# Kernel tuning notes

Hardware: AMD Instinct MI355X
Metric: run time of the kernel (lower is better)

Reference implementation:

```python
import jax, jax.numpy as jnp
import numpy as np

B, S, K, N = 4, 2048, 4096, 4096   # batch, seq, infeatures, outfeatures
GROUP = 128                        # quantization group size along K
N_OUT = 128                        # outlier features (last columns of x)


def setup_inputs() -> dict:
    key = jax.random.key(0)
    ks = jax.random.split(key, 6)
    x = jax.random.normal(ks[0], (B, S, K), dtype=jnp.float32)
    # unpacked 4-bit integer weights in [0, 16)
    qweight = jax.random.randint(ks[1], (N, K), 0, 16, dtype=jnp.int32)
    # per-group scales and scaled zeros: [numgroup, N] = [K//GROUP, N]
    scales = jax.random.uniform(ks[2], (K // GROUP, N), dtype=jnp.float32, minval=0.005, maxval=0.02)
    # scaled_zeros = -zeros * scales in the original pack(); keep them negative-ish
    scaled_zeros = -jax.random.uniform(ks[3], (K // GROUP, N), dtype=jnp.float32, minval=0.0, maxval=0.16)
    oweight = jax.random.normal(ks[4], (N, N_OUT), dtype=jnp.float32) * 0.02
    bias = jax.random.normal(ks[5], (N,), dtype=jnp.float32) * 0.02
    return {"x": x, "qweight": qweight, "scales": scales,
            "scaled_zeros": scaled_zeros, "oweight": oweight, "bias": bias}


def reference(x, qweight, scales, scaled_zeros, oweight, bias):
    # gemm_4bit: dequantize W[n,k] = q[n,k]*scales[k//G, n] + scaled_zeros[k//G, n]
    g = x.shape[-1] // scales.shape[0]
    scales_full = jnp.repeat(scales, g, axis=0).T        # [N, K]
    zeros_full = jnp.repeat(scaled_zeros, g, axis=0).T   # [N, K]
    W = qweight.astype(scales.dtype) * scales_full + zeros_full  # [N, K]
    y = jnp.einsum('bsk,nk->bsn', x, W)
    # fused outlier fp16 linear on the last N_OUT input features + bias
    n_out = oweight.shape[1]
    y = y + jnp.einsum('bso,no->bsn', x[..., -n_out:], oweight) + bias
    return y
```

## Files before the change

### kernel.cpp

```cpp
#include <hip/hip_runtime.h>

#define K_ 4096
#define N_ 4096
#define M_ 8192
#define NOUT_ 128

typedef __bf16 bf16x8 __attribute__((ext_vector_type(8)));
typedef float f32x4 __attribute__((ext_vector_type(4)));
typedef unsigned short ushort8 __attribute__((ext_vector_type(8)));

__device__ __forceinline__ unsigned short f2bf(float f) {
  unsigned u = __builtin_bit_cast(unsigned, f);
  u += 0x7fffu + ((u >> 16) & 1u);
  return (unsigned short)(u >> 16);
}

__global__ void cvt_x_kernel(const float4* __restrict__ x4, ushort8* __restrict__ xb) {
  const int t = blockIdx.x * 256 + threadIdx.x;
  float4 a = x4[2 * t];
  float4 b = x4[2 * t + 1];
  ushort8 o;
  o[0] = f2bf(a.x); o[1] = f2bf(a.y); o[2] = f2bf(a.z); o[3] = f2bf(a.w);
  o[4] = f2bf(b.x); o[5] = f2bf(b.y); o[6] = f2bf(b.z); o[7] = f2bf(b.w);
  xb[t] = o;
}

__global__ void dequant_kernel(const int4* __restrict__ q4,
                               const float* __restrict__ scales,
                               const float* __restrict__ zeros,
                               const float* __restrict__ ow,
                               ushort8* __restrict__ wb) {
  const int t = blockIdx.x * 256 + threadIdx.x;
  const int n = t >> 9;
  const int k = (t & 511) << 3;
  const int g = k >> 7;
  const float s = scales[g * N_ + n];
  const float z = zeros[g * N_ + n];
  int4 qa = q4[2 * t], qb = q4[2 * t + 1];
  float f[8];
  f[0] = qa.x * s + z; f[1] = qa.y * s + z; f[2] = qa.z * s + z; f[3] = qa.w * s + z;
  f[4] = qb.x * s + z; f[5] = qb.y * s + z; f[6] = qb.z * s + z; f[7] = qb.w * s + z;
  if (k >= K_ - NOUT_) {
    const float4* o4 = (const float4*)(ow + n * NOUT_ + (k - (K_ - NOUT_)));
    float4 oa = o4[0], ob = o4[1];
    f[0] += oa.x; f[1] += oa.y; f[2] += oa.z; f[3] += oa.w;
    f[4] += ob.x; f[5] += ob.y; f[6] += ob.z; f[7] += ob.w;
  }
  ushort8 r;
  #pragma unroll
  for (int i = 0; i < 8; ++i) r[i] = f2bf(f[i]);
  wb[t] = r;
}

__global__ __launch_bounds__(256, 3) void gemm_kernel(
    const unsigned short* __restrict__ xb,
    const unsigned short* __restrict__ wb,
    const float* __restrict__ bias,
    float* __restrict__ out) {
  __shared__ char sA[16384];
  __shared__ char sB[16384];

  const int tid  = threadIdx.x;
  const int w    = tid >> 6;
  const int lane = tid & 63;
  const int q    = lane >> 4;
  const int l16  = lane & 15;
  const int x7   = l16 & 7;
  const int wr   = w >> 1;
  const int wc   = w & 1;

  const int m0 = blockIdx.y * 128;
  const int n0 = blockIdx.x * 128;

  const unsigned short* gA[4];
  const unsigned short* gB[4];
  char* ldsA[4];
  char* ldsB[4];
  #pragma unroll
  for (int i = 0; i < 4; ++i) {
    const int o  = i * 4096 + w * 1024 + lane * 16;
    const int r  = o >> 7;
    const int cs = (o >> 4) & 7;
    const int cg = cs ^ (r & 7);
    gA[i] = xb + (size_t)(m0 + r) * K_ + cg * 8;
    gB[i] = wb + (size_t)(n0 + r) * K_ + cg * 8;
    ldsA[i] = sA + i * 4096 + w * 1024;
    ldsB[i] = sB + i * 4096 + w * 1024;
  }

  const char* pA = sA + (wr * 64 + l16) * 128;
  const char* pB = sB + (wc * 64 + l16) * 128;
  const int slot0 = ((0 + q) ^ x7) * 16;
  const int slot1 = ((4 + q) ^ x7) * 16;

  f32x4 acc[4][4] = {};

  for (int kt = 0; kt < K_ / 64; ++kt) {
    const int kof = kt * 64;
    #pragma unroll
    for (int i = 0; i < 4; ++i)
      __builtin_amdgcn_global_load_lds(
          (__attribute__((address_space(1))) void*)(gA[i] + kof),
          (__attribute__((address_space(3))) void*)ldsA[i], 16, 0, 0);
    #pragma unroll
    for (int i = 0; i < 4; ++i)
      __builtin_amdgcn_global_load_lds(
          (__attribute__((address_space(1))) void*)(gB[i] + kof),
          (__attribute__((address_space(3))) void*)ldsB[i], 16, 0, 0);
    __syncthreads();

    #pragma unroll
    for (int s = 0; s < 2; ++s) {
      const int slot = s ? slot1 : slot0;
      bf16x8 a[4], b[4];
      #pragma unroll
      for (int i = 0; i < 4; ++i)
        a[i] = *(const bf16x8*)(pA + i * 2048 + slot);
      #pragma unroll
      for (int j = 0; j < 4; ++j)
        b[j] = *(const bf16x8*)(pB + j * 2048 + slot);
      #pragma unroll
      for (int i = 0; i < 4; ++i)
        #pragma unroll
        for (int j = 0; j < 4; ++j)
          acc[i][j] = __builtin_amdgcn_mfma_f32_16x16x32_bf16(a[i], b[j], acc[i][j], 0, 0, 0);
    }
    __syncthreads();
  }

  float bv[4];
  #pragma unroll
  for (int j = 0; j < 4; ++j)
    bv[j] = bias[n0 + wc * 64 + j * 16 + l16];

  #pragma unroll
  for (int i = 0; i < 4; ++i) {
    const int mrow = m0 + wr * 64 + i * 16 + q * 4;
    #pragma unroll
    for (int j = 0; j < 4; ++j) {
      const int n = n0 + wc * 64 + j * 16 + l16;
      float* op = out + (size_t)mrow * N_ + n;
      #pragma unroll
      for (int r = 0; r < 4; ++r)
        op[(size_t)r * N_] = acc[i][j][r] + bv[j];
    }
  }
}

extern "C" void kernel_launch(void* const* d_in, const int* in_sizes, int n_in,
                              void* d_out, int out_size, void* d_ws, size_t ws_size,
                              hipStream_t stream) {
  const float* x      = (const float*)d_in[0];
  const int*   qw     = (const int*)d_in[1];
  const float* scales = (const float*)d_in[2];
  const float* zeros  = (const float*)d_in[3];
  const float* ow     = (const float*)d_in[4];
  const float* bias   = (const float*)d_in[5];
  float* out = (float*)d_out;

  unsigned short* xb = (unsigned short*)d_ws;
  unsigned short* wb = xb + (size_t)M_ * K_;

  cvt_x_kernel<<<(M_ * K_ / 8) / 256, 256, 0, stream>>>((const float4*)x, (ushort8*)xb);
  dequant_kernel<<<(N_ * K_ / 8) / 256, 256, 0, stream>>>((const int4*)qw, scales, zeros, ow,
                                                          (ushort8*)wb);
  dim3 grid(N_ / 128, M_ / 128);
  gemm_kernel<<<grid, 256, 0, stream>>>(xb, wb, bias, out);
}
```

Before: 531.6 us.

## Use 256x256 tiles with double-buffered LDS prefetch and 8-wave MFMA schedule

Tiles grow from 128x128 with 4 waves to 256x256 with 8 waves, and LDS becomes double-buffered so the next K-tile loads through global_load_lds while MFMAs run on the current one. The compute phase is split into four sub-phases separated by barriers and setprio hints, and block IDs are remapped for L2 locality. This targets global load latency and LDS traffic per MFMA. The cost is 128KB of LDS per block, which limits occupancy, more registers for the accumulators, and many extra barriers.

After: 552.5 us. 1.04x slower.

```diff
diff --git a/kernel.cpp b/kernel.cpp
--- a/kernel.cpp
+++ b/kernel.cpp
@@ -4,6 +4,7 @@
 #define N_ 4096
 #define M_ 8192
 #define NOUT_ 128
+#define NT_ (K_ / 64)
 
 typedef __bf16 bf16x8 __attribute__((ext_vector_type(8)));
 typedef float f32x4 __attribute__((ext_vector_type(4)));
@@ -52,80 +53,145 @@
   wb[t] = r;
 }
 
-__global__ __launch_bounds__(256, 3) void gemm_kernel(
+#define STAGE(dA, dB, kof)                                                          \
+  do {                                                                              \
+    _Pragma("unroll") for (int i_ = 0; i_ < 4; ++i_)                                \
+        __builtin_amdgcn_global_load_lds(                                           \
+            (__attribute__((address_space(1))) void*)(gA[i_] + (kof)),              \
+            (__attribute__((address_space(3))) void*)((dA) + aoff[i_]), 16, 0, 0);  \
+    _Pragma("unroll") for (int i_ = 0; i_ < 4; ++i_)                                \
+        __builtin_amdgcn_global_load_lds(                                           \
+            (__attribute__((address_space(1))) void*)(gB[i_] + (kof)),              \
+            (__attribute__((address_space(3))) void*)((dB) + aoff[i_]), 16, 0, 0);  \
+  } while (0)
+
+__global__ __launch_bounds__(512, 2) void gemm_kernel(
     const unsigned short* __restrict__ xb,
     const unsigned short* __restrict__ wb,
     const float* __restrict__ bias,
     float* __restrict__ out) {
-  __shared__ char sA[16384];
-  __shared__ char sB[16384];
+  __shared__ __attribute__((aligned(16))) char lds[131072];
 
   const int tid  = threadIdx.x;
   const int w    = tid >> 6;
   const int lane = tid & 63;
   const int q    = lane >> 4;
   const int l16  = lane & 15;
-  const int x7   = l16 & 7;
-  const int wr   = w >> 1;
-  const int wc   = w & 1;
-
-  const int m0 = blockIdx.y * 128;
-  const int n0 = blockIdx.x * 128;
+  const int wr   = w >> 2;
+  const int wc   = w & 3;
+
+  const int id  = blockIdx.y * 16 + blockIdx.x;
+  const int id2 = (id & 7) * 64 + (id >> 3);
+  const int m0  = (id2 >> 4) * 256;
+  const int n0  = (id2 & 15) * 256;
 
   const unsigned short* gA[4];
   const unsigned short* gB[4];
-  char* ldsA[4];
-  char* ldsB[4];
+  int aoff[4];
   #pragma unroll
   for (int i = 0; i < 4; ++i) {
-    const int o  = i * 4096 + w * 1024 + lane * 16;
+    const int o  = i * 8192 + w * 1024 + lane * 16;
     const int r  = o >> 7;
     const int cs = (o >> 4) & 7;
     const int cg = cs ^ (r & 7);
     gA[i] = xb + (size_t)(m0 + r) * K_ + cg * 8;
     gB[i] = wb + (size_t)(n0 + r) * K_ + cg * 8;
-    ldsA[i] = sA + i * 4096 + w * 1024;
-    ldsB[i] = sB + i * 4096 + w * 1024;
-  }
-
-  const char* pA = sA + (wr * 64 + l16) * 128;
-  const char* pB = sB + (wc * 64 + l16) * 128;
-  const int slot0 = ((0 + q) ^ x7) * 16;
-  const int slot1 = ((4 + q) ^ x7) * 16;
-
-  f32x4 acc[4][4] = {};
-
-  for (int kt = 0; kt < K_ / 64; ++kt) {
-    const int kof = kt * 64;
-    #pragma unroll
-    for (int i = 0; i < 4; ++i)
-      __builtin_amdgcn_global_load_lds(
-          (__attribute__((address_space(1))) void*)(gA[i] + kof),
-          (__attribute__((address_space(3))) void*)ldsA[i], 16, 0, 0);
-    #pragma unroll
-    for (int i = 0; i < 4; ++i)
-      __builtin_amdgcn_global_load_lds(
-          (__attribute__((address_space(1))) void*)(gB[i] + kof),
-          (__attribute__((address_space(3))) void*)ldsB[i], 16, 0, 0);
-    __syncthreads();
-
-    #pragma unroll
-    for (int s = 0; s < 2; ++s) {
-      const int slot = s ? slot1 : slot0;
-      bf16x8 a[4], b[4];
-      #pragma unroll
-      for (int i = 0; i < 4; ++i)
-        a[i] = *(const bf16x8*)(pA + i * 2048 + slot);
-      #pragma unroll
-      for (int j = 0; j < 4; ++j)
-        b[j] = *(const bf16x8*)(pB + j * 2048 + slot);
-      #pragma unroll
-      for (int i = 0; i < 4; ++i)
-        #pragma unroll
-        for (int j = 0; j < 4; ++j)
-          acc[i][j] = __builtin_amdgcn_mfma_f32_16x16x32_bf16(a[i], b[j], acc[i][j], 0, 0, 0);
-    }
-    __syncthreads();
+    aoff[i] = i * 8192 + w * 1024;
+  }
+
+  const char* pA0 = lds + (wr * 128 + l16) * 128;
+  const char* pB0 = lds + 65536 + (wc * 64 + l16) * 128;
+  const int sl0 = ((0 + q) ^ (l16 & 7)) * 16;
+  const int sl1 = ((4 + q) ^ (l16 & 7)) * 16;
+
+  f32x4 acc[8][4] = {};
+
+  STAGE((char*)lds, (char*)lds + 65536, 0);
+
+  for (int t = 0; t < NT_; ++t) {
+    const int curo = (t & 1) * 32768;
+    const char* cA = pA0 + curo;
+    const char* cB = pB0 + curo;
+
+    if (t + 1 < NT_) {
+      char* dA = (char*)lds + (((t + 1) & 1) * 32768);
+      char* dB = (char*)lds + 65536 + (((t + 1) & 1) * 32768);
+      STAGE(dA, dB, (t + 1) * 64);
+      asm volatile("s_waitcnt vmcnt(8)" ::: "memory");
+    } else {
+      asm volatile("s_waitcnt vmcnt(0)" ::: "memory");
+    }
+    __builtin_amdgcn_s_barrier();
+    __builtin_amdgcn_sched_barrier(0);
+
+    bf16x8 a[4][2], b0[2][2], b1[2][2];
+
+    #pragma unroll
+    for (int f = 0; f < 4; ++f) {
+      a[f][0] = *(const bf16x8*)(cA + f * 2048 + sl0);
+      a[f][1] = *(const bf16x8*)(cA + f * 2048 + sl1);
+    }
+    #pragma unroll
+    for (int j = 0; j < 2; ++j) {
+      b0[j][0] = *(const bf16x8*)(cB + j * 2048 + sl0);
+      b0[j][1] = *(const bf16x8*)(cB + j * 2048 + sl1);
+    }
+    __builtin_amdgcn_s_barrier();
+    __builtin_amdgcn_s_setprio(1);
+    #pragma unroll
+    for (int f = 0; f < 4; ++f)
+      #pragma unroll
+      for (int j = 0; j < 2; ++j) {
+        acc[f][j] = __builtin_amdgcn_mfma_f32_16x16x32_bf16(a[f][0], b0[j][0], acc[f][j], 0, 0, 0);
+        acc[f][j] = __builtin_amdgcn_mfma_f32_16x16x32_bf16(a[f][1], b0[j][1], acc[f][j], 0, 0, 0);
+      }
+    __builtin_amdgcn_s_setprio(0);
+    __builtin_amdgcn_s_barrier();
+
+    #pragma unroll
+    for (int j = 0; j < 2; ++j) {
+      b1[j][0] = *(const bf16x8*)(cB + (2 + j) * 2048 + sl0);
+      b1[j][1] = *(const bf16x8*)(cB + (2 + j) * 2048 + sl1);
+    }
+    __builtin_amdgcn_s_barrier();
+    __builtin_amdgcn_s_setprio(1);
+    #pragma unroll
+    for (int f = 0; f < 4; ++f)
+      #pragma unroll
+      for (int j = 0; j < 2; ++j) {
+        acc[f][2 + j] = __builtin_amdgcn_mfma_f32_16x16x32_bf16(a[f][0], b1[j][0], acc[f][2 + j], 0, 0, 0);
+        acc[f][2 + j] = __builtin_amdgcn_mfma_f32_16x16x32_bf16(a[f][1], b1[j][1], acc[f][2 + j], 0, 0, 0);
+      }
+    __builtin_amdgcn_s_setprio(0);
+    __builtin_amdgcn_s_barrier();
+
+    #pragma unroll
+    for (int f = 0; f < 4; ++f) {
+      a[f][0] = *(const bf16x8*)(cA + (4 + f) * 2048 + sl0);
+      a[f][1] = *(const bf16x8*)(cA + (4 + f) * 2048 + sl1);
+    }
+    __builtin_amdgcn_s_barrier();
+    __builtin_amdgcn_s_setprio(1);
+    #pragma unroll
+    for (int f = 0; f < 4; ++f)
+      #pragma unroll
+      for (int j = 0; j < 2; ++j) {
+        acc[4 + f][j] = __builtin_amdgcn_mfma_f32_16x16x32_bf16(a[f][0], b0[j][0], acc[4 + f][j], 0, 0, 0);
+        acc[4 + f][j] = __builtin_amdgcn_mfma_f32_16x16x32_bf16(a[f][1], b0[j][1], acc[4 + f][j], 0, 0, 0);
+      }
+    __builtin_amdgcn_s_setprio(0);
+    __builtin_amdgcn_s_barrier();
+
+    __builtin_amdgcn_s_setprio(1);
+    #pragma unroll
+    for (int f = 0; f < 4; ++f)
+      #pragma unroll
+      for (int j = 0; j < 2; ++j) {
+        acc[4 + f][2 + j] = __builtin_amdgcn_mfma_f32_16x16x32_bf16(a[f][0], b1[j][0], acc[4 + f][2 + j], 0, 0, 0);
+        acc[4 + f][2 + j] = __builtin_amdgcn_mfma_f32_16x16x32_bf16(a[f][1], b1[j][1], acc[4 + f][2 + j], 0, 0, 0);
+      }
+    __builtin_amdgcn_s_setprio(0);
+    __builtin_amdgcn_s_barrier();
   }
 
   float bv[4];
@@ -134,8 +200,8 @@
     bv[j] = bias[n0 + wc * 64 + j * 16 + l16];
 
   #pragma unroll
-  for (int i = 0; i < 4; ++i) {
-    const int mrow = m0 + wr * 64 + i * 16 + q * 4;
+  for (int i = 0; i < 8; ++i) {
+    const int mrow = m0 + wr * 128 + i * 16 + q * 4;
     #pragma unroll
     for (int j = 0; j < 4; ++j) {
       const int n = n0 + wc * 64 + j * 16 + l16;
@@ -164,6 +230,6 @@
   cvt_x_kernel<<<(M_ * K_ / 8) / 256, 256, 0, stream>>>((const float4*)x, (ushort8*)xb);
   dequant_kernel<<<(N_ * K_ / 8) / 256, 256, 0, stream>>>((const int4*)qw, scales, zeros, ow,
                                                           (ushort8*)wb);
-  dim3 grid(N_ / 128, M_ / 128);
-  gemm_kernel<<<grid, 256, 0, stream>>>(xb, wb, bias, out);
-}
+  dim3 grid(N_ / 256, M_ / 256);
+  gemm_kernel<<<grid, 512, 0, stream>>>(xb, wb, bias, out);
+}
```
